# Kernel optimization log

Measured on AMD Instinct MI355X. Metric: run time of the kernel, lower is better.

Reference implementation:

```python
import jax, jax.numpy as jnp
import numpy as np

VOCAB = 30000
N_NODES = 10000
N_EDGES = 160000
D = 1024


def setup_inputs() -> dict:
    key = jax.random.key(0)
    ks = jax.random.split(key, 10)
    s = 1.0 / np.sqrt(D)
    return {
        "node": jax.random.randint(ks[0], (N_NODES,), 0, VOCAB),
        "src": jax.random.randint(ks[1], (N_EDGES,), 0, N_NODES),
        "dst": jax.random.randint(ks[2], (N_EDGES,), 0, N_NODES),
        "emb": jax.random.normal(ks[3], (VOCAB, D), jnp.float32),
        "W1_self": jax.random.uniform(ks[4], (D, D), jnp.float32, -s, s),
        "W1_neigh": jax.random.uniform(ks[5], (D, D), jnp.float32, -s, s),
        "b1": jax.random.uniform(ks[6], (D,), jnp.float32, -s, s),
        "W2_self": jax.random.uniform(ks[7], (D, D), jnp.float32, -s, s),
        "W2_neigh": jax.random.uniform(ks[8], (D, D), jnp.float32, -s, s),
        "b2": jax.random.uniform(ks[9], (D,), jnp.float32, -s, s),
    }


def _sage_conv(h, src, dst, W_self, W_neigh, b):
    # DGL SAGEConv 'mean': mean over in-neighbors (src -> dst), 0 for isolated dst
    n = h.shape[0]
    deg = jax.ops.segment_sum(jnp.ones((src.shape[0],), h.dtype), dst, num_segments=n)
    agg = jax.ops.segment_sum(h[src], dst, num_segments=n)  # [n, D]
    h_neigh = agg / jnp.maximum(deg, 1.0)[:, None]
    # rst = fc_self(h) + fc_neigh(h_neigh); fc_self has no bias in DGL
    return h @ W_self + h_neigh @ W_neigh + b


def reference(node, src, dst, emb, W1_self, W1_neigh, b1, W2_self, W2_neigh, b2):
    x = emb[node]  # [N_NODES, D] embedding lookup
    h = jax.nn.relu(_sage_conv(x, src, dst, W1_self, W1_neigh, b1))
    return _sage_conv(h, src, dst, W2_self, W2_neigh, b2)
```

## Files before the change

kernel.cpp:

```cpp
#include <hip/hip_runtime.h>
#include <hip/hip_bf16.h>

#define N_NODES 10000
#define N_EDGES 160000
#define DD 1024
#define KCAT 2048
#define MPAD 10240
#define MTILES 79
#define NTILES 8
#define NBLK (MTILES * NTILES)

#define AGG_BLOCKS 1000
#define AGG_WPS 500

typedef __attribute__((ext_vector_type(8))) __bf16 bf16x8;
typedef __attribute__((ext_vector_type(4))) __bf16 bf16x4;
typedef __attribute__((ext_vector_type(4))) float f32x4;

__device__ inline void gload_lds16(const void* g, void* l) {
  __builtin_amdgcn_global_load_lds((const __attribute__((address_space(1))) void*)g,
                                   (__attribute__((address_space(3))) void*)l, 16, 0, 0);
}

__global__ __launch_bounds__(256) void k_hist(const int* __restrict__ dst,
                                              int* __restrict__ deg) {
  int e = blockIdx.x * 256 + threadIdx.x;
  if (e < N_EDGES) atomicAdd(&deg[dst[e]], 1);
}

__global__ __launch_bounds__(1024) void k_scan(const int* __restrict__ deg,
                                               int* __restrict__ off) {
  int t = threadIdx.x;
  int base_i = t * 10;
  int loc[10];
  int sum = 0;
#pragma unroll
  for (int j = 0; j < 10; ++j) {
    int idx = base_i + j;
    int v = (idx < N_NODES) ? deg[idx] : 0;
    loc[j] = sum;
    sum += v;
  }
  int lane = t & 63, w = t >> 6;
  int inc = sum;
#pragma unroll
  for (int d = 1; d < 64; d <<= 1) {
    int y = __shfl_up(inc, d);
    if (lane >= d) inc += y;
  }
  __shared__ int wtot[16];
  __shared__ int wpre[16];
  if (lane == 63) wtot[w] = inc;
  __syncthreads();
  if (t == 0) {
    int c = 0;
    for (int k = 0; k < 16; ++k) { wpre[k] = c; c += wtot[k]; }
    off[N_NODES] = c;
  }
  __syncthreads();
  int tbase = wpre[w] + (inc - sum);
#pragma unroll
  for (int j = 0; j < 10; ++j) {
    int idx = base_i + j;
    if (idx < N_NODES) off[idx] = tbase + loc[j];
  }
}

__global__ __launch_bounds__(256) void k_fill(const int* __restrict__ src,
                                              const int* __restrict__ dst,
                                              const int* __restrict__ off,
                                              int* __restrict__ cursor,
                                              int* __restrict__ eidx) {
  int e = blockIdx.x * 256 + threadIdx.x;
  if (e < N_EDGES) {
    int d = dst[e];
    int pos = atomicAdd(&cursor[d], 1);
    eidx[off[d] + pos] = src[e];
  }
}

__global__ __launch_bounds__(256) void k_embed(const int* __restrict__ node,
                                               const float* __restrict__ emb,
                                               __bf16* __restrict__ xcat) {
  int i = blockIdx.x;
  int t = threadIdx.x;
  float4 v = ((const float4*)(emb + (size_t)node[i] * DD))[t];
  bf16x4 o;
  o[0] = (__bf16)v.x; o[1] = (__bf16)v.y; o[2] = (__bf16)v.z; o[3] = (__bf16)v.w;
  *(bf16x4*)(xcat + (size_t)i * KCAT + t * 4) = o;
}

__global__ __launch_bounds__(256) void k_wconv(const float* __restrict__ Ws,
                                               const float* __restrict__ Wn,
                                               __bf16* __restrict__ Wt) {
  __shared__ float tile[32][33];
  int k0 = blockIdx.x * 32;
  int c0 = blockIdx.y * 32;
  for (int i = threadIdx.y; i < 32; i += 8) {
    int k = k0 + i, c = c0 + threadIdx.x;
    float v = (k < DD) ? Ws[(size_t)k * DD + c] : Wn[(size_t)(k - DD) * DD + c];
    tile[i][threadIdx.x] = v;
  }
  __syncthreads();
  for (int i = threadIdx.y; i < 32; i += 8) {
    int c = c0 + i, k = k0 + threadIdx.x;
    Wt[(size_t)c * KCAT + k] = (__bf16)tile[threadIdx.x][i];
  }
}

__global__ __launch_bounds__(256) void k_agg(__bf16* __restrict__ buf,
                                             const int* __restrict__ off,
                                             const int* __restrict__ eidx) {
  const int s    = blockIdx.x & 7;
  const int q    = blockIdx.x >> 3;
  const int lane = threadIdx.x & 63;
  const int w    = threadIdx.x >> 6;
  const int wid  = q * 4 + w;
  const size_t colb = (size_t)s * 128 + lane * 2;

  for (int n = wid; n < N_NODES; n += AGG_WPS) {
    int s0 = off[n], e0 = off[n + 1];
    float a0 = 0.f, a1 = 0.f, b0 = 0.f, b1 = 0.f;
    int i = s0;
    for (; i + 2 <= e0; i += 2) {
      const __bf16* r0 = buf + (size_t)eidx[i] * KCAT + colb;
      const __bf16* r1 = buf + (size_t)eidx[i + 1] * KCAT + colb;
      a0 += (float)r0[0]; a1 += (float)r0[1];
      b0 += (float)r1[0]; b1 += (float)r1[1];
    }
    if (i < e0) {
      const __bf16* r0 = buf + (size_t)eidx[i] * KCAT + colb;
      a0 += (float)r0[0]; a1 += (float)r0[1];
    }
    float inv = 1.0f / fmaxf((float)(e0 - s0), 1.0f);
    __bf16 o0 = (__bf16)((a0 + b0) * inv);
    __bf16 o1 = (__bf16)((a1 + b1) * inv);
    __bf16* dstp = buf + (size_t)n * KCAT + DD + colb;
    dstp[0] = o0; dstp[1] = o1;
  }
}

template <int MODE>
__global__ __launch_bounds__(256, 2) void k_gemm(const __bf16* __restrict__ A,
                                                 const __bf16* __restrict__ Bt,
                                                 const float* __restrict__ bias,
                                                 float* __restrict__ Cf,
                                                 __bf16* __restrict__ Cb,
                                                 int Mreal) {
  __shared__ char smem[65536];
  const int tid  = threadIdx.x;
  const int lane = tid & 63;
  const int w    = tid >> 6;
  const int wr   = w >> 1, wc = w & 1;
  const int b  = blockIdx.x;
  const int l  = (b & 7) * MTILES + (b >> 3);
  const int m0 = (l >> 3) * 128;
  const int n0 = (l & 7) * 128;

  f32x4 acc[4][4];
#pragma unroll
  for (int m = 0; m < 4; ++m)
#pragma unroll
    for (int n = 0; n < 4; ++n) acc[m][n] = f32x4{0.f, 0.f, 0.f, 0.f};

  int sr[4], sk[4];
#pragma unroll
  for (int i = 0; i < 4; ++i) {
    int G = (4 * w + i) * 64 + lane;
    int E = G ^ ((G >> 3) & 7);
    sr[i] = E >> 3;
    sk[i] = (E & 7) * 8;
  }

  auto stage = [&](int buf, int kt) {
    char* As = smem + buf * 32768;
    char* Bs = As + 16384;
#pragma unroll
    for (int i = 0; i < 4; ++i) {
      gload_lds16(A + (size_t)(m0 + sr[i]) * KCAT + (kt + sk[i]), As + (4 * w + i) * 1024);
      gload_lds16(Bt + (size_t)(n0 + sr[i]) * KCAT + (kt + sk[i]), Bs + (4 * w + i) * 1024);
    }
  };

  auto compute = [&](int buf) {
    char* As = smem + buf * 32768;
    char* Bs = As + 16384;
#pragma unroll
    for (int kk = 0; kk < 64; kk += 32) {
      const int koff = kk + ((lane >> 4) * 8);
      bf16x8 af[4], bfr[4];
#pragma unroll
      for (int m = 0; m < 4; ++m) {
        int r = wr * 64 + m * 16 + (lane & 15);
        int byte = ((r * 64 + koff) * 2) ^ ((r & 7) << 4);
        af[m] = *(const bf16x8*)(As + byte);
      }
#pragma unroll
      for (int n = 0; n < 4; ++n) {
        int c = wc * 64 + n * 16 + (lane & 15);
        int byte = ((c * 64 + koff) * 2) ^ ((c & 7) << 4);
        bfr[n] = *(const bf16x8*)(Bs + byte);
      }
#pragma unroll
      for (int m = 0; m < 4; ++m)
#pragma unroll
        for (int n = 0; n < 4; ++n)
          acc[m][n] = __builtin_amdgcn_mfma_f32_16x16x32_bf16(af[m], bfr[n], acc[m][n], 0, 0, 0);
    }
  };

  stage(0, 0);
  __syncthreads();
  int cur = 0;
  for (int kt = 0; kt < KCAT; kt += 64) {
    if (kt + 64 < KCAT) stage(cur ^ 1, kt + 64);
    compute(cur);
    __syncthreads();
    cur ^= 1;
  }

  const int rb = m0 + wr * 64;
  const int cb = n0 + wc * 64;
#pragma unroll
  for (int m = 0; m < 4; ++m) {
#pragma unroll
    for (int n = 0; n < 4; ++n) {
      int c = cb + n * 16 + (lane & 15);
      float bv = bias[c];
#pragma unroll
      for (int j = 0; j < 4; ++j) {
        int r = rb + m * 16 + (lane >> 4) * 4 + j;
        if (r < Mreal) {
          float v = acc[m][n][j] + bv;
          if constexpr (MODE == 1) {
            v = fmaxf(v, 0.f);
            Cb[(size_t)r * KCAT + c] = (__bf16)v;
          } else {
            Cf[(size_t)r * DD + c] = v;
          }
        }
      }
    }
  }
}

extern "C" void kernel_launch(void* const* d_in, const int* in_sizes, int n_in,
                              void* d_out, int out_size, void* d_ws, size_t ws_size,
                              hipStream_t stream) {
  const int*   node = (const int*)d_in[0];
  const int*   srcv = (const int*)d_in[1];
  const int*   dstv = (const int*)d_in[2];
  const float* emb  = (const float*)d_in[3];
  const float* W1s  = (const float*)d_in[4];
  const float* W1n  = (const float*)d_in[5];
  const float* b1   = (const float*)d_in[6];
  const float* W2s  = (const float*)d_in[7];
  const float* W2n  = (const float*)d_in[8];
  const float* b2   = (const float*)d_in[9];
  float* out = (float*)d_out;

  char* ws = (char*)d_ws;
  __bf16* xcat = (__bf16*)ws; ws += (size_t)MPAD * KCAT * 2;
  __bf16* hcat = (__bf16*)ws; ws += (size_t)MPAD * KCAT * 2;
  __bf16* Wt1  = (__bf16*)ws; ws += (size_t)DD * KCAT * 2;
  __bf16* Wt2  = (__bf16*)ws; ws += (size_t)DD * KCAT * 2;
  int* deg    = (int*)ws; ws += 40960;
  int* cursor = (int*)ws; ws += 40960;
  int* off    = (int*)ws; ws += 40960;
  int* eidx   = (int*)ws; ws += (size_t)N_EDGES * 4;

  hipMemsetAsync(deg, 0, 2 * 40960, stream);

  k_hist<<<(N_EDGES + 255) / 256, 256, 0, stream>>>(dstv, deg);
  k_scan<<<1, 1024, 0, stream>>>(deg, off);
  k_fill<<<(N_EDGES + 255) / 256, 256, 0, stream>>>(srcv, dstv, off, cursor, eidx);

  k_embed<<<N_NODES, 256, 0, stream>>>(node, emb, xcat);
  k_wconv<<<dim3(64, 32), dim3(32, 8), 0, stream>>>(W1s, W1n, Wt1);
  k_wconv<<<dim3(64, 32), dim3(32, 8), 0, stream>>>(W2s, W2n, Wt2);

  k_agg<<<AGG_BLOCKS, 256, 0, stream>>>(xcat, off, eidx);
  k_gemm<1><<<NBLK, 256, 0, stream>>>(xcat, Wt1, b1, nullptr, hcat, N_NODES);

  k_agg<<<AGG_BLOCKS, 256, 0, stream>>>(hcat, off, eidx);
  k_gemm<0><<<NBLK, 256, 0, stream>>>(hcat, Wt2, b2, out, nullptr, N_NODES);
}
```

Before: 518.7 us.

## Vectorize neighbor aggregation, coalesce scan, merge weight conversions, double agg grid

The aggregation kernel now has each lane load 8 bf16 values (16 bytes) per neighbor row, with four lane groups handling different edges in parallel and combining their partial sums through cross-lane shuffles. This replaces the old scalar 2-element loads and is meant to raise memory-level parallelism on the gather. The prefix scan now reads in a coalesced chunked order, carrying the running total across chunks. The two weight-conversion launches are merged into one grid that uses the z dimension, and the aggregation grid is doubled.

```diff
diff --git a/kernel.cpp b/kernel.cpp
--- a/kernel.cpp
+++ b/kernel.cpp
@@ -10,8 +10,8 @@
 #define NTILES 8
 #define NBLK (MTILES * NTILES)
 
-#define AGG_BLOCKS 1000
-#define AGG_WPS 500
+#define AGG_BLOCKS 2000
+#define AGG_WPS 1000
 
 typedef __attribute__((ext_vector_type(8))) __bf16 bf16x8;
 typedef __attribute__((ext_vector_type(4))) __bf16 bf16x4;
@@ -30,40 +30,32 @@
 
 __global__ __launch_bounds__(1024) void k_scan(const int* __restrict__ deg,
                                                int* __restrict__ off) {
-  int t = threadIdx.x;
-  int base_i = t * 10;
-  int loc[10];
-  int sum = 0;
-#pragma unroll
-  for (int j = 0; j < 10; ++j) {
-    int idx = base_i + j;
-    int v = (idx < N_NODES) ? deg[idx] : 0;
-    loc[j] = sum;
-    sum += v;
-  }
-  int lane = t & 63, w = t >> 6;
-  int inc = sum;
-#pragma unroll
-  for (int d = 1; d < 64; d <<= 1) {
-    int y = __shfl_up(inc, d);
-    if (lane >= d) inc += y;
-  }
   __shared__ int wtot[16];
   __shared__ int wpre[16];
-  if (lane == 63) wtot[w] = inc;
+  __shared__ int carry_s;
+  int t = threadIdx.x, lane = t & 63, w = t >> 6;
+  if (t == 0) carry_s = 0;
   __syncthreads();
-  if (t == 0) {
-    int c = 0;
-    for (int k = 0; k < 16; ++k) { wpre[k] = c; c += wtot[k]; }
-    off[N_NODES] = c;
-  }
-  __syncthreads();
-  int tbase = wpre[w] + (inc - sum);
-#pragma unroll
-  for (int j = 0; j < 10; ++j) {
-    int idx = base_i + j;
-    if (idx < N_NODES) off[idx] = tbase + loc[j];
-  }
+  for (int c = 0; c < 10; ++c) {
+    int idx = c * 1024 + t;
+    int v = (idx < N_NODES) ? deg[idx] : 0;
+    int inc = v;
+#pragma unroll
+    for (int d = 1; d < 64; d <<= 1) {
+      int y = __shfl_up(inc, d);
+      if (lane >= d) inc += y;
+    }
+    if (lane == 63) wtot[w] = inc;
+    __syncthreads();
+    if (t == 0) {
+      int acc = carry_s;
+      for (int k = 0; k < 16; ++k) { wpre[k] = acc; acc += wtot[k]; }
+      carry_s = acc;
+    }
+    __syncthreads();
+    if (idx < N_NODES) off[idx] = wpre[w] + (inc - v);
+  }
+  if (t == 0) off[N_NODES] = carry_s;
 }
 
 __global__ __launch_bounds__(256) void k_fill(const int* __restrict__ src,
@@ -90,9 +82,15 @@
   *(bf16x4*)(xcat + (size_t)i * KCAT + t * 4) = o;
 }
 
-__global__ __launch_bounds__(256) void k_wconv(const float* __restrict__ Ws,
-                                               const float* __restrict__ Wn,
-                                               __bf16* __restrict__ Wt) {
+__global__ __launch_bounds__(256) void k_wconv(const float* __restrict__ W1s,
+                                               const float* __restrict__ W1n,
+                                               const float* __restrict__ W2s,
+                                               const float* __restrict__ W2n,
+                                               __bf16* __restrict__ Wt1,
+                                               __bf16* __restrict__ Wt2) {
+  const float* Ws = blockIdx.z ? W2s : W1s;
+  const float* Wn = blockIdx.z ? W2n : W1n;
+  __bf16* Wt = blockIdx.z ? Wt2 : Wt1;
   __shared__ float tile[32][33];
   int k0 = blockIdx.x * 32;
   int c0 = blockIdx.y * 32;
@@ -115,28 +113,51 @@
   const int q    = blockIdx.x >> 3;
   const int lane = threadIdx.x & 63;
   const int w    = threadIdx.x >> 6;
+  const int g    = lane >> 4;
+  const int l    = lane & 15;
   const int wid  = q * 4 + w;
-  const size_t colb = (size_t)s * 128 + lane * 2;
+  const size_t colb = (size_t)s * 128 + l * 8;
 
   for (int n = wid; n < N_NODES; n += AGG_WPS) {
-    int s0 = off[n], e0 = off[n + 1];
-    float a0 = 0.f, a1 = 0.f, b0 = 0.f, b1 = 0.f;
+    const int s0 = off[n], e0 = off[n + 1];
+    float acc[8];
+#pragma unroll
+    for (int j = 0; j < 8; ++j) acc[j] = 0.f;
     int i = s0;
-    for (; i + 2 <= e0; i += 2) {
-      const __bf16* r0 = buf + (size_t)eidx[i] * KCAT + colb;
-      const __bf16* r1 = buf + (size_t)eidx[i + 1] * KCAT + colb;
-      a0 += (float)r0[0]; a1 += (float)r0[1];
-      b0 += (float)r1[0]; b1 += (float)r1[1];
-    }
-    if (i < e0) {
-      const __bf16* r0 = buf + (size_t)eidx[i] * KCAT + colb;
-      a0 += (float)r0[0]; a1 += (float)r0[1];
-    }
-    float inv = 1.0f / fmaxf((float)(e0 - s0), 1.0f);
-    __bf16 o0 = (__bf16)((a0 + b0) * inv);
-    __bf16 o1 = (__bf16)((a1 + b1) * inv);
-    __bf16* dstp = buf + (size_t)n * KCAT + DD + colb;
-    dstp[0] = o0; dstp[1] = o1;
+    for (; i + 8 <= e0; i += 8) {
+      int eA = eidx[i + g];
+      int eB = eidx[i + 4 + g];
+      bf16x8 vA = *(const bf16x8*)(buf + (size_t)eA * KCAT + colb);
+      bf16x8 vB = *(const bf16x8*)(buf + (size_t)eB * KCAT + colb);
+#pragma unroll
+      for (int j = 0; j < 8; ++j) acc[j] += (float)vA[j] + (float)vB[j];
+    }
+    if (i + 4 <= e0) {
+      int eA = eidx[i + g];
+      bf16x8 vA = *(const bf16x8*)(buf + (size_t)eA * KCAT + colb);
+#pragma unroll
+      for (int j = 0; j < 8; ++j) acc[j] += (float)vA[j];
+      i += 4;
+    }
+    int rem = e0 - i;
+    if (g < rem) {
+      int eA = eidx[i + g];
+      bf16x8 vA = *(const bf16x8*)(buf + (size_t)eA * KCAT + colb);
+#pragma unroll
+      for (int j = 0; j < 8; ++j) acc[j] += (float)vA[j];
+    }
+#pragma unroll
+    for (int j = 0; j < 8; ++j) {
+      acc[j] += __shfl_xor(acc[j], 16);
+      acc[j] += __shfl_xor(acc[j], 32);
+    }
+    if (g == 0) {
+      float inv = 1.0f / fmaxf((float)(e0 - s0), 1.0f);
+      bf16x8 o;
+#pragma unroll
+      for (int j = 0; j < 8; ++j) o[j] = (__bf16)(acc[j] * inv);
+      *(bf16x8*)(buf + (size_t)n * KCAT + DD + colb) = o;
+    }
   }
 }
 
@@ -276,8 +297,7 @@
   k_fill<<<(N_EDGES + 255) / 256, 256, 0, stream>>>(srcv, dstv, off, cursor, eidx);
 
   k_embed<<<N_NODES, 256, 0, stream>>>(node, emb, xcat);
-  k_wconv<<<dim3(64, 32), dim3(32, 8), 0, stream>>>(W1s, W1n, Wt1);
-  k_wconv<<<dim3(64, 32), dim3(32, 8), 0, stream>>>(W2s, W2n, Wt2);
+  k_wconv<<<dim3(64, 32, 2), dim3(32, 8), 0, stream>>>(W1s, W1n, W2s, W2n, Wt1, Wt2);
 
   k_agg<<<AGG_BLOCKS, 256, 0, stream>>>(xcat, off, eidx);
   k_gemm<1><<<NBLK, 256, 0, stream>>>(xcat, Wt1, b1, nullptr, hcat, N_NODES);
```

After: 435.8 us. -16.0%, faster.
